# Performance work log

Measured on AMD Instinct MI355X. Metric: run time of the kernel, lower is better.

Reference implementation:

```python
import jax, jax.numpy as jnp
import numpy as np

TEMP = 0.2
N_IT = 10
P = 1


def setup_inputs() -> dict:
    key = jax.random.key(0)
    N, M = 8192, 8192
    k1, _ = jax.random.split(key)
    cdist = jax.random.uniform(k1, (N, M), dtype=jnp.float32)
    A = jnp.ones((N,), dtype=jnp.float32) / N  # uniform source density
    B = jnp.ones((M,), dtype=jnp.float32) / M  # uniform target density
    return {"cdist": cdist, "A": A, "B": B}


def reference(cdist, A, B):
    N, M = cdist.shape
    # C = (cdist - cdist.min()) / cdist.std(); torch std is unbiased (ddof=1)
    C = (cdist - cdist.min()) / jnp.std(cdist, ddof=1)
    # p == 1 -> no power applied
    Q = jnp.exp(-C / TEMP)
    Q = Q / Q.sum()

    def body(i, carry):
        U, V = carry
        # T implicit as U[:,None] * Q * V; first iter T == Q since U=V=1
        T = U[:, None] * Q * V[None, :]
        V = V * (B / T.sum(axis=0))
        T = U[:, None] * Q * V[None, :]
        U = U * (A / T.sum(axis=1))
        return (U, V)

    U0 = jnp.ones((N,), dtype=cdist.dtype)
    V0 = jnp.ones((M,), dtype=cdist.dtype)
    U, V = jax.lax.fori_loop(0, N_IT, body, (U0, V0))
    T = U[:, None] * Q * V[None, :]
    return T
```

## Files before the change

### kernel.cpp

```cpp
#include <hip/hip_runtime.h>
#include <hip/hip_fp16.h>

#define TEMP_ 0.2
#define NITER 10

typedef _Float16 half_t;
struct __align__(8)  H4 { half_t h[4]; };
struct __align__(16) H8 { half_t h[8]; };

__device__ __forceinline__ float wsum(float v){
#pragma unroll
  for (int o = 32; o > 0; o >>= 1) v += __shfl_down(v, o, 64);
  return v;
}
__device__ __forceinline__ double wsumd(double v){
#pragma unroll
  for (int o = 32; o > 0; o >>= 1) v += __shfl_down(v, o, 64);
  return v;
}
__device__ __forceinline__ float wmin(float v){
#pragma unroll
  for (int o = 32; o > 0; o >>= 1) v = fminf(v, __shfl_down(v, o, 64));
  return v;
}

__device__ __forceinline__ unsigned fenc(float f){
  unsigned u = __float_as_uint(f);
  return (u & 0x80000000u) ? ~u : (u | 0x80000000u);
}
__device__ __forceinline__ float fdec(unsigned u){
  return (u & 0x80000000u) ? __uint_as_float(u & 0x7FFFFFFFu) : __uint_as_float(~u);
}

__device__ __forceinline__ void get_stats(const double* __restrict__ sums,
                                          const unsigned* __restrict__ minbits,
                                          long long NM, float& cmin, float& kscale){
  double s  = sums[0];
  double ss = sums[1];
  double mean = s / (double)NM;
  double var  = (ss - mean * s) / (double)(NM - 1);
  cmin  = fdec(*minbits);
  kscale = (float)(1.0 / (sqrt(var) * TEMP_));
}

__global__ void k_init(double* __restrict__ sums, double* __restrict__ Ssum,
                       unsigned* __restrict__ minbits, float* __restrict__ colsum, int M){
  int i = blockIdx.x * blockDim.x + threadIdx.x;
  if (i == 0){ sums[0] = 0.0; sums[1] = 0.0; *Ssum = 0.0; *minbits = 0xFFFFFFFFu; }
  if (i < M) colsum[i] = 0.f;
}

__global__ __launch_bounds__(256) void k_reduce(const float* __restrict__ cd, long long n4,
                                                double* __restrict__ sums,
                                                unsigned* __restrict__ minbits){
  const float4* c4 = (const float4*)cd;
  long long i0 = (long long)blockIdx.x * blockDim.x + threadIdx.x;
  long long stride = (long long)gridDim.x * blockDim.x;
  double s = 0.0, ss = 0.0;
  float  fs = 0.f, fss = 0.f;
  float  mn = __int_as_float(0x7F800000);
  int cnt = 0;
  for (long long i = i0; i < n4; i += stride){
    float4 v = c4[i];
    mn = fminf(mn, fminf(fminf(v.x, v.y), fminf(v.z, v.w)));
    fs  += (v.x + v.y) + (v.z + v.w);
    fss += v.x*v.x + v.y*v.y + v.z*v.z + v.w*v.w;
    if (++cnt == 8){ s += fs; ss += fss; fs = 0.f; fss = 0.f; cnt = 0; }
  }
  s += fs; ss += fss;
  s = wsumd(s); ss = wsumd(ss); mn = wmin(mn);
  __shared__ double lds[8];
  __shared__ float  ldm[4];
  int lane = threadIdx.x & 63, wid = threadIdx.x >> 6;
  if (lane == 0){ lds[wid] = s; lds[4 + wid] = ss; ldm[wid] = mn; }
  __syncthreads();
  if (threadIdx.x == 0){
    unsafeAtomicAdd(&sums[0], lds[0] + lds[1] + lds[2] + lds[3]);
    unsafeAtomicAdd(&sums[1], lds[4] + lds[5] + lds[6] + lds[7]);
    atomicMin(minbits, fenc(fminf(fminf(ldm[0], ldm[1]), fminf(ldm[2], ldm[3]))));
  }
}

__global__ __launch_bounds__(256) void k_expcol(const float* __restrict__ cd, half_t* __restrict__ E,
                                                const double* __restrict__ sums,
                                                const unsigned* __restrict__ minbits,
                                                float* __restrict__ colsum, double* __restrict__ Ssum,
                                                int N, int M){
  float cmin, kscale;
  get_stats(sums, minbits, (long long)N * M, cmin, kscale);
  int c0 = blockIdx.x * 1024 + threadIdx.x * 4;
  int r0 = blockIdx.y * 64;
  float a0 = 0.f, a1 = 0.f, a2 = 0.f, a3 = 0.f;
#pragma unroll 4
  for (int r = 0; r < 64; ++r){
    long long idx = (long long)(r0 + r) * M + c0;
    float4 v = *(const float4*)(cd + idx);
    float e0 = __expf((cmin - v.x) * kscale);
    float e1 = __expf((cmin - v.y) * kscale);
    float e2 = __expf((cmin - v.z) * kscale);
    float e3 = __expf((cmin - v.w) * kscale);
    H4 o; o.h[0] = (half_t)e0; o.h[1] = (half_t)e1; o.h[2] = (half_t)e2; o.h[3] = (half_t)e3;
    *(H4*)(E + idx) = o;
    a0 += e0; a1 += e1; a2 += e2; a3 += e3;
  }
  unsafeAtomicAdd(&colsum[c0 + 0], a0);
  unsafeAtomicAdd(&colsum[c0 + 1], a1);
  unsafeAtomicAdd(&colsum[c0 + 2], a2);
  unsafeAtomicAdd(&colsum[c0 + 3], a3);
  float tot = wsum((a0 + a1) + (a2 + a3));
  __shared__ float lt[4];
  int lane = threadIdx.x & 63, wid = threadIdx.x >> 6;
  if (lane == 0) lt[wid] = tot;
  __syncthreads();
  if (threadIdx.x == 0) unsafeAtomicAdd(Ssum, (double)(lt[0] + lt[1] + lt[2] + lt[3]));
}

__global__ void k_v(const float* __restrict__ B, const float* __restrict__ colsum,
                    const double* __restrict__ Ssum, float* __restrict__ v, int M){
  int j = blockIdx.x * blockDim.x + threadIdx.x;
  if (j < M) v[j] = (float)((double)B[j] * (*Ssum) / (double)colsum[j]);
}

__global__ __launch_bounds__(256) void k_row(const half_t* __restrict__ E, const float* __restrict__ v,
                                             float* __restrict__ rowsum, int M){
  int t = threadIdx.x;
  int r0 = blockIdx.x * 8;
  float vr[32];
#pragma unroll
  for (int k = 0; k < 4; ++k){
    int c = k * 2048 + t * 8;
    float4 a = *(const float4*)(v + c);
    float4 b = *(const float4*)(v + c + 4);
    vr[k*8+0] = a.x; vr[k*8+1] = a.y; vr[k*8+2] = a.z; vr[k*8+3] = a.w;
    vr[k*8+4] = b.x; vr[k*8+5] = b.y; vr[k*8+6] = b.z; vr[k*8+7] = b.w;
  }
  __shared__ float lds[4][8];
  int lane = t & 63, wid = t >> 6;
  for (int r = 0; r < 8; ++r){
    const half_t* Er = E + (long long)(r0 + r) * M;
    float p = 0.f;
#pragma unroll
    for (int k = 0; k < 4; ++k){
      H8 hh = *(const H8*)(Er + k * 2048 + t * 8);
      p += (float)hh.h[0]*vr[k*8+0] + (float)hh.h[1]*vr[k*8+1]
         + (float)hh.h[2]*vr[k*8+2] + (float)hh.h[3]*vr[k*8+3]
         + (float)hh.h[4]*vr[k*8+4] + (float)hh.h[5]*vr[k*8+5]
         + (float)hh.h[6]*vr[k*8+6] + (float)hh.h[7]*vr[k*8+7];
    }
    p = wsum(p);
    if (lane == 0) lds[wid][r] = p;
  }
  __syncthreads();
  if (t < 8) rowsum[r0 + t] = lds[0][t] + lds[1][t] + lds[2][t] + lds[3][t];
}

__global__ void k_u(const float* __restrict__ A, const float* __restrict__ rowsum,
                    const double* __restrict__ Ssum, float* __restrict__ u,
                    float* __restrict__ colsum, int N, int M){
  int i = blockIdx.x * blockDim.x + threadIdx.x;
  if (i < N) u[i] = (float)((double)A[i] * (*Ssum) / (double)rowsum[i]);
  if (i < M) colsum[i] = 0.f;
}

__global__ __launch_bounds__(256) void k_col(const half_t* __restrict__ E, const float* __restrict__ u,
                                             float* __restrict__ colsum, int M){
  int c0 = blockIdx.x * 1024 + threadIdx.x * 4;
  int r0 = blockIdx.y * 64;
  float a0 = 0.f, a1 = 0.f, a2 = 0.f, a3 = 0.f;
#pragma unroll 4
  for (int r = 0; r < 64; ++r){
    int row = r0 + r;
    float ur = u[row];
    H4 hh = *(const H4*)(E + (long long)row * M + c0);
    a0 += ur * (float)hh.h[0];
    a1 += ur * (float)hh.h[1];
    a2 += ur * (float)hh.h[2];
    a3 += ur * (float)hh.h[3];
  }
  unsafeAtomicAdd(&colsum[c0 + 0], a0);
  unsafeAtomicAdd(&colsum[c0 + 1], a1);
  unsafeAtomicAdd(&colsum[c0 + 2], a2);
  unsafeAtomicAdd(&colsum[c0 + 3], a3);
}

__global__ __launch_bounds__(256) void k_final(const float* __restrict__ cd,
                                               const float* __restrict__ u, const float* __restrict__ v,
                                               const double* __restrict__ sums,
                                               const unsigned* __restrict__ minbits,
                                               const double* __restrict__ Ssum,
                                               float* __restrict__ T, int N, int M){
  float cmin, kscale;
  get_stats(sums, minbits, (long long)N * M, cmin, kscale);
  float invS = (float)(1.0 / (*Ssum));
  int t = threadIdx.x;
  int r0 = blockIdx.x * 8;
  float vr[32];
#pragma unroll
  for (int k = 0; k < 4; ++k){
    int c = k * 2048 + t * 8;
    float4 a = *(const float4*)(v + c);
    float4 b = *(const float4*)(v + c + 4);
    vr[k*8+0] = a.x * invS; vr[k*8+1] = a.y * invS; vr[k*8+2] = a.z * invS; vr[k*8+3] = a.w * invS;
    vr[k*8+4] = b.x * invS; vr[k*8+5] = b.y * invS; vr[k*8+6] = b.z * invS; vr[k*8+7] = b.w * invS;
  }
  for (int r = 0; r < 8; ++r){
    int row = r0 + r;
    float ur = u[row];
#pragma unroll
    for (int k = 0; k < 4; ++k){
      long long idx = (long long)row * M + k * 2048 + t * 8;
      float4 a = *(const float4*)(cd + idx);
      float4 b = *(const float4*)(cd + idx + 4);
      float4 oa, ob;
      oa.x = ur * vr[k*8+0] * __expf((cmin - a.x) * kscale);
      oa.y = ur * vr[k*8+1] * __expf((cmin - a.y) * kscale);
      oa.z = ur * vr[k*8+2] * __expf((cmin - a.z) * kscale);
      oa.w = ur * vr[k*8+3] * __expf((cmin - a.w) * kscale);
      ob.x = ur * vr[k*8+4] * __expf((cmin - b.x) * kscale);
      ob.y = ur * vr[k*8+5] * __expf((cmin - b.y) * kscale);
      ob.z = ur * vr[k*8+6] * __expf((cmin - b.z) * kscale);
      ob.w = ur * vr[k*8+7] * __expf((cmin - b.w) * kscale);
      *(float4*)(T + idx) = oa;
      *(float4*)(T + idx + 4) = ob;
    }
  }
}

extern "C" void kernel_launch(void* const* d_in, const int* in_sizes, int n_in,
                              void* d_out, int out_size, void* d_ws, size_t ws_size,
                              hipStream_t stream){
  const float* cd = (const float*)d_in[0];
  const float* A  = (const float*)d_in[1];
  const float* B  = (const float*)d_in[2];
  int N = in_sizes[1];
  int M = in_sizes[2];
  float*  T = (float*)d_out;
  half_t* E = (half_t*)d_out;

  char* ws = (char*)d_ws;
  double*   sums    = (double*)ws;
  double*   Ssum    = (double*)(ws + 16);
  unsigned* minbits = (unsigned*)(ws + 24);
  float*    colsum  = (float*)(ws + 32);
  float*    rowsum  = colsum + M;
  float*    u       = rowsum + N;
  float*    v       = u + N;

  int mx = (N > M) ? N : M;
  long long n4 = (long long)N * M / 4;

  k_init<<<(mx + 255) / 256, 256, 0, stream>>>(sums, Ssum, minbits, colsum, M);
  k_reduce<<<2048, 256, 0, stream>>>(cd, n4, sums, minbits);
  k_expcol<<<dim3(M / 1024, N / 64), 256, 0, stream>>>(cd, E, sums, minbits, colsum, Ssum, N, M);

  for (int it = 0; it < NITER; ++it){
    if (it > 0) k_col<<<dim3(M / 1024, N / 64), 256, 0, stream>>>(E, u, colsum, M);
    k_v<<<(M + 255) / 256, 256, 0, stream>>>(B, colsum, Ssum, v, M);
    k_row<<<N / 8, 256, 0, stream>>>(E, v, rowsum, M);
    k_u<<<(mx + 255) / 256, 256, 0, stream>>>(A, rowsum, Ssum, u, colsum, N, M);
  }
  k_final<<<N / 8, 256, 0, stream>>>(cd, u, v, sums, minbits, Ssum, T, N, M);
}
```

Measured before the change: 1.206 ms.

## Fuse scaling kernels into row/column passes and build final output from fp16 E

Drops the separate k_v and k_u kernels. v is computed on the fly from the column sums in a shared load_vr helper, and u is computed at the end of the row pass (k_rp). Column sums now ping-pong between two buffers, and the zeroing for the next iteration is folded into the column pass (k_cp), which also caches u in LDS. Column and exp kernels move to 8-wide fp16 vectors, and reciprocals use the fast hardware rcp instead of double division. The final output is built from the fp16 E matrix for three quarters of the rows, in an order that respects E aliasing the output buffer, with nontemporal stores. This trades output precision (fp16 E, approximate rcp) for fewer launches and less fp32 traffic.

Result: slower. 1.353 ms (+12.2%).

```diff
diff --git a/kernel.cpp b/kernel.cpp
--- a/kernel.cpp
+++ b/kernel.cpp
@@ -1,12 +1,14 @@
 #include <hip/hip_runtime.h>
-#include <hip/hip_fp16.h>
 
 #define TEMP_ 0.2
 #define NITER 10
 
+
 typedef _Float16 half_t;
-struct __align__(8)  H4 { half_t h[4]; };
 struct __align__(16) H8 { half_t h[8]; };
+typedef float floatx4 __attribute__((ext_vector_type(4)));
+
+__device__ __forceinline__ float fast_rcp(float x){ return __builtin_amdgcn_rcpf(x); }
 
 __device__ __forceinline__ float wsum(float v){
 #pragma unroll
@@ -43,11 +45,33 @@
   kscale = (float)(1.0 / (sqrt(var) * TEMP_));
 }
 
+__device__ __forceinline__ void load_vr(const float* __restrict__ cs,
+                                        const float* __restrict__ B,
+                                        float S, int t, float* vr){
+#pragma unroll
+  for (int k = 0; k < 4; ++k){
+    int c = k * 2048 + t * 8;
+    float4 ca = *(const float4*)(cs + c);
+    float4 cb = *(const float4*)(cs + c + 4);
+    float4 ba = *(const float4*)(B + c);
+    float4 bb = *(const float4*)(B + c + 4);
+    vr[k*8+0] = ba.x * S * fast_rcp(ca.x);
+    vr[k*8+1] = ba.y * S * fast_rcp(ca.y);
+    vr[k*8+2] = ba.z * S * fast_rcp(ca.z);
+    vr[k*8+3] = ba.w * S * fast_rcp(ca.w);
+    vr[k*8+4] = bb.x * S * fast_rcp(cb.x);
+    vr[k*8+5] = bb.y * S * fast_rcp(cb.y);
+    vr[k*8+6] = bb.z * S * fast_rcp(cb.z);
+    vr[k*8+7] = bb.w * S * fast_rcp(cb.w);
+  }
+}
+
 __global__ void k_init(double* __restrict__ sums, double* __restrict__ Ssum,
-                       unsigned* __restrict__ minbits, float* __restrict__ colsum, int M){
+                       unsigned* __restrict__ minbits,
+                       float* __restrict__ c0, float* __restrict__ c1, int M){
   int i = blockIdx.x * blockDim.x + threadIdx.x;
   if (i == 0){ sums[0] = 0.0; sums[1] = 0.0; *Ssum = 0.0; *minbits = 0xFFFFFFFFu; }
-  if (i < M) colsum[i] = 0.f;
+  if (i < M){ c0[i] = 0.f; c1[i] = 0.f; }
 }
 
 __global__ __launch_bounds__(256) void k_reduce(const float* __restrict__ cd, long long n4,
@@ -88,121 +112,166 @@
                                                 int N, int M){
   float cmin, kscale;
   get_stats(sums, minbits, (long long)N * M, cmin, kscale);
-  int c0 = blockIdx.x * 1024 + threadIdx.x * 4;
+  int t = threadIdx.x;
+  int c0 = blockIdx.x * 2048 + t * 8;
   int r0 = blockIdx.y * 64;
-  float a0 = 0.f, a1 = 0.f, a2 = 0.f, a3 = 0.f;
+  float a0=0.f,a1=0.f,a2=0.f,a3=0.f,a4=0.f,a5=0.f,a6=0.f,a7=0.f;
 #pragma unroll 4
   for (int r = 0; r < 64; ++r){
     long long idx = (long long)(r0 + r) * M + c0;
-    float4 v = *(const float4*)(cd + idx);
-    float e0 = __expf((cmin - v.x) * kscale);
-    float e1 = __expf((cmin - v.y) * kscale);
-    float e2 = __expf((cmin - v.z) * kscale);
-    float e3 = __expf((cmin - v.w) * kscale);
-    H4 o; o.h[0] = (half_t)e0; o.h[1] = (half_t)e1; o.h[2] = (half_t)e2; o.h[3] = (half_t)e3;
-    *(H4*)(E + idx) = o;
-    a0 += e0; a1 += e1; a2 += e2; a3 += e3;
-  }
-  unsafeAtomicAdd(&colsum[c0 + 0], a0);
-  unsafeAtomicAdd(&colsum[c0 + 1], a1);
-  unsafeAtomicAdd(&colsum[c0 + 2], a2);
-  unsafeAtomicAdd(&colsum[c0 + 3], a3);
-  float tot = wsum((a0 + a1) + (a2 + a3));
+    float4 va = *(const float4*)(cd + idx);
+    float4 vb = *(const float4*)(cd + idx + 4);
+    float e0 = __expf((cmin - va.x) * kscale);
+    float e1 = __expf((cmin - va.y) * kscale);
+    float e2 = __expf((cmin - va.z) * kscale);
+    float e3 = __expf((cmin - va.w) * kscale);
+    float e4 = __expf((cmin - vb.x) * kscale);
+    float e5 = __expf((cmin - vb.y) * kscale);
+    float e6 = __expf((cmin - vb.z) * kscale);
+    float e7 = __expf((cmin - vb.w) * kscale);
+    H8 o;
+    o.h[0]=(half_t)e0; o.h[1]=(half_t)e1; o.h[2]=(half_t)e2; o.h[3]=(half_t)e3;
+    o.h[4]=(half_t)e4; o.h[5]=(half_t)e5; o.h[6]=(half_t)e6; o.h[7]=(half_t)e7;
+    *(H8*)(E + idx) = o;
+    a0+=e0; a1+=e1; a2+=e2; a3+=e3; a4+=e4; a5+=e5; a6+=e6; a7+=e7;
+  }
+  unsafeAtomicAdd(&colsum[c0+0], a0);
+  unsafeAtomicAdd(&colsum[c0+1], a1);
+  unsafeAtomicAdd(&colsum[c0+2], a2);
+  unsafeAtomicAdd(&colsum[c0+3], a3);
+  unsafeAtomicAdd(&colsum[c0+4], a4);
+  unsafeAtomicAdd(&colsum[c0+5], a5);
+  unsafeAtomicAdd(&colsum[c0+6], a6);
+  unsafeAtomicAdd(&colsum[c0+7], a7);
+  float tot = wsum(((a0+a1)+(a2+a3)) + ((a4+a5)+(a6+a7)));
   __shared__ float lt[4];
-  int lane = threadIdx.x & 63, wid = threadIdx.x >> 6;
+  int lane = t & 63, wid = t >> 6;
   if (lane == 0) lt[wid] = tot;
   __syncthreads();
-  if (threadIdx.x == 0) unsafeAtomicAdd(Ssum, (double)(lt[0] + lt[1] + lt[2] + lt[3]));
-}
-
-__global__ void k_v(const float* __restrict__ B, const float* __restrict__ colsum,
-                    const double* __restrict__ Ssum, float* __restrict__ v, int M){
-  int j = blockIdx.x * blockDim.x + threadIdx.x;
-  if (j < M) v[j] = (float)((double)B[j] * (*Ssum) / (double)colsum[j]);
-}
-
-__global__ __launch_bounds__(256) void k_row(const half_t* __restrict__ E, const float* __restrict__ v,
-                                             float* __restrict__ rowsum, int M){
+  if (t == 0) unsafeAtomicAdd(Ssum, (double)((lt[0] + lt[1]) + (lt[2] + lt[3])));
+}
+
+__global__ __launch_bounds__(256) void k_rp(const half_t* __restrict__ E,
+                                            const float* __restrict__ cs,
+                                            const float* __restrict__ B,
+                                            const float* __restrict__ A,
+                                            const double* __restrict__ Ssum,
+                                            float* __restrict__ u, int M){
   int t = threadIdx.x;
   int r0 = blockIdx.x * 8;
+  float S = (float)(*Ssum);
   float vr[32];
-#pragma unroll
-  for (int k = 0; k < 4; ++k){
-    int c = k * 2048 + t * 8;
-    float4 a = *(const float4*)(v + c);
-    float4 b = *(const float4*)(v + c + 4);
-    vr[k*8+0] = a.x; vr[k*8+1] = a.y; vr[k*8+2] = a.z; vr[k*8+3] = a.w;
-    vr[k*8+4] = b.x; vr[k*8+5] = b.y; vr[k*8+6] = b.z; vr[k*8+7] = b.w;
-  }
-  __shared__ float lds[4][8];
-  int lane = t & 63, wid = t >> 6;
+  load_vr(cs, B, S, t, vr);
+  float acc[8];
+  const half_t* Eb = E + (long long)r0 * M;
+#pragma unroll
   for (int r = 0; r < 8; ++r){
-    const half_t* Er = E + (long long)(r0 + r) * M;
     float p = 0.f;
 #pragma unroll
     for (int k = 0; k < 4; ++k){
-      H8 hh = *(const H8*)(Er + k * 2048 + t * 8);
+      H8 hh = *(const H8*)(Eb + (long long)r * M + k * 2048 + t * 8);
       p += (float)hh.h[0]*vr[k*8+0] + (float)hh.h[1]*vr[k*8+1]
          + (float)hh.h[2]*vr[k*8+2] + (float)hh.h[3]*vr[k*8+3]
          + (float)hh.h[4]*vr[k*8+4] + (float)hh.h[5]*vr[k*8+5]
          + (float)hh.h[6]*vr[k*8+6] + (float)hh.h[7]*vr[k*8+7];
     }
-    p = wsum(p);
+    acc[r] = p;
+  }
+  __shared__ float lds[4][8];
+  int lane = t & 63, wid = t >> 6;
+#pragma unroll
+  for (int r = 0; r < 8; ++r){
+    float p = wsum(acc[r]);
     if (lane == 0) lds[wid][r] = p;
   }
   __syncthreads();
-  if (t < 8) rowsum[r0 + t] = lds[0][t] + lds[1][t] + lds[2][t] + lds[3][t];
-}
-
-__global__ void k_u(const float* __restrict__ A, const float* __restrict__ rowsum,
-                    const double* __restrict__ Ssum, float* __restrict__ u,
-                    float* __restrict__ colsum, int N, int M){
-  int i = blockIdx.x * blockDim.x + threadIdx.x;
-  if (i < N) u[i] = (float)((double)A[i] * (*Ssum) / (double)rowsum[i]);
-  if (i < M) colsum[i] = 0.f;
-}
-
-__global__ __launch_bounds__(256) void k_col(const half_t* __restrict__ E, const float* __restrict__ u,
-                                             float* __restrict__ colsum, int M){
-  int c0 = blockIdx.x * 1024 + threadIdx.x * 4;
+  if (t < 8){
+    float rs = (lds[0][t] + lds[1][t]) + (lds[2][t] + lds[3][t]);
+    u[r0 + t] = A[r0 + t] * S * fast_rcp(rs);
+  }
+}
+
+__global__ __launch_bounds__(256) void k_cp(const half_t* __restrict__ E,
+                                            const float* __restrict__ u,
+                                            float* __restrict__ cs_next,
+                                            float* __restrict__ cs_zero, int M){
+  int t = threadIdx.x;
+  int c0 = blockIdx.x * 2048 + t * 8;
   int r0 = blockIdx.y * 64;
-  float a0 = 0.f, a1 = 0.f, a2 = 0.f, a3 = 0.f;
-#pragma unroll 4
+  int bid = blockIdx.y * gridDim.x + blockIdx.x;
+  int z = bid * 16 + t;
+  if (t < 16 && z < M) cs_zero[z] = 0.f;
+  __shared__ float ul[64];
+  if (t < 64) ul[t] = u[r0 + t];
+  __syncthreads();
+  float a0=0.f,a1=0.f,a2=0.f,a3=0.f,a4=0.f,a5=0.f,a6=0.f,a7=0.f;
+#pragma unroll 8
   for (int r = 0; r < 64; ++r){
-    int row = r0 + r;
-    float ur = u[row];
-    H4 hh = *(const H4*)(E + (long long)row * M + c0);
+    float ur = ul[r];
+    H8 hh = *(const H8*)(E + (long long)(r0 + r) * M + c0);
     a0 += ur * (float)hh.h[0];
     a1 += ur * (float)hh.h[1];
     a2 += ur * (float)hh.h[2];
     a3 += ur * (float)hh.h[3];
-  }
-  unsafeAtomicAdd(&colsum[c0 + 0], a0);
-  unsafeAtomicAdd(&colsum[c0 + 1], a1);
-  unsafeAtomicAdd(&colsum[c0 + 2], a2);
-  unsafeAtomicAdd(&colsum[c0 + 3], a3);
-}
-
-__global__ __launch_bounds__(256) void k_final(const float* __restrict__ cd,
-                                               const float* __restrict__ u, const float* __restrict__ v,
-                                               const double* __restrict__ sums,
-                                               const unsigned* __restrict__ minbits,
-                                               const double* __restrict__ Ssum,
-                                               float* __restrict__ T, int N, int M){
+    a4 += ur * (float)hh.h[4];
+    a5 += ur * (float)hh.h[5];
+    a6 += ur * (float)hh.h[6];
+    a7 += ur * (float)hh.h[7];
+  }
+  unsafeAtomicAdd(&cs_next[c0+0], a0);
+  unsafeAtomicAdd(&cs_next[c0+1], a1);
+  unsafeAtomicAdd(&cs_next[c0+2], a2);
+  unsafeAtomicAdd(&cs_next[c0+3], a3);
+  unsafeAtomicAdd(&cs_next[c0+4], a4);
+  unsafeAtomicAdd(&cs_next[c0+5], a5);
+  unsafeAtomicAdd(&cs_next[c0+6], a6);
+  unsafeAtomicAdd(&cs_next[c0+7], a7);
+}
+
+__global__ __launch_bounds__(256) void k_final_E(const half_t* __restrict__ E,
+                                                 const float* __restrict__ u,
+                                                 const float* __restrict__ cs,
+                                                 const float* __restrict__ B,
+                                                 float* __restrict__ T, int r_base, int M){
+  int t = threadIdx.x;
+  int r0 = r_base + blockIdx.x * 8;
+  float vr[32];
+  load_vr(cs, B, 1.0f, t, vr);
+  for (int r = 0; r < 8; ++r){
+    int row = r0 + r;
+    float ur = u[row];
+#pragma unroll
+    for (int k = 0; k < 4; ++k){
+      long long idx = (long long)row * M + k * 2048 + t * 8;
+      H8 hh = *(const H8*)(E + idx);
+      floatx4 oa, ob;
+      oa.x = ur * vr[k*8+0] * (float)hh.h[0];
+      oa.y = ur * vr[k*8+1] * (float)hh.h[1];
+      oa.z = ur * vr[k*8+2] * (float)hh.h[2];
+      oa.w = ur * vr[k*8+3] * (float)hh.h[3];
+      ob.x = ur * vr[k*8+4] * (float)hh.h[4];
+      ob.y = ur * vr[k*8+5] * (float)hh.h[5];
+      ob.z = ur * vr[k*8+6] * (float)hh.h[6];
+      ob.w = ur * vr[k*8+7] * (float)hh.h[7];
+      __builtin_nontemporal_store(oa, (floatx4*)(T + idx));
+      __builtin_nontemporal_store(ob, (floatx4*)(T + idx + 4));
+    }
+  }
+}
+
+__global__ __launch_bounds__(256) void k_final_cd(const float* __restrict__ cd,
+                                                  const float* __restrict__ u,
+                                                  const float* __restrict__ cs,
+                                                  const float* __restrict__ B,
+                                                  const double* __restrict__ sums,
+                                                  const unsigned* __restrict__ minbits,
+                                                  float* __restrict__ T, int N, int M){
   float cmin, kscale;
   get_stats(sums, minbits, (long long)N * M, cmin, kscale);
-  float invS = (float)(1.0 / (*Ssum));
   int t = threadIdx.x;
   int r0 = blockIdx.x * 8;
   float vr[32];
-#pragma unroll
-  for (int k = 0; k < 4; ++k){
-    int c = k * 2048 + t * 8;
-    float4 a = *(const float4*)(v + c);
-    float4 b = *(const float4*)(v + c + 4);
-    vr[k*8+0] = a.x * invS; vr[k*8+1] = a.y * invS; vr[k*8+2] = a.z * invS; vr[k*8+3] = a.w * invS;
-    vr[k*8+4] = b.x * invS; vr[k*8+5] = b.y * invS; vr[k*8+6] = b.z * invS; vr[k*8+7] = b.w * invS;
-  }
+  load_vr(cs, B, 1.0f, t, vr);
   for (int r = 0; r < 8; ++r){
     int row = r0 + r;
     float ur = u[row];
@@ -211,7 +280,7 @@
       long long idx = (long long)row * M + k * 2048 + t * 8;
       float4 a = *(const float4*)(cd + idx);
       float4 b = *(const float4*)(cd + idx + 4);
-      float4 oa, ob;
+      floatx4 oa, ob;
       oa.x = ur * vr[k*8+0] * __expf((cmin - a.x) * kscale);
       oa.y = ur * vr[k*8+1] * __expf((cmin - a.y) * kscale);
       oa.z = ur * vr[k*8+2] * __expf((cmin - a.z) * kscale);
@@ -220,8 +289,8 @@
       ob.y = ur * vr[k*8+5] * __expf((cmin - b.y) * kscale);
       ob.z = ur * vr[k*8+6] * __expf((cmin - b.z) * kscale);
       ob.w = ur * vr[k*8+7] * __expf((cmin - b.w) * kscale);
-      *(float4*)(T + idx) = oa;
-      *(float4*)(T + idx + 4) = ob;
+      __builtin_nontemporal_store(oa, (floatx4*)(T + idx));
+      __builtin_nontemporal_store(ob, (floatx4*)(T + idx + 4));
     }
   }
 }
@@ -241,23 +310,26 @@
   double*   sums    = (double*)ws;
   double*   Ssum    = (double*)(ws + 16);
   unsigned* minbits = (unsigned*)(ws + 24);
-  float*    colsum  = (float*)(ws + 32);
-  float*    rowsum  = colsum + M;
-  float*    u       = rowsum + N;
-  float*    v       = u + N;
-
-  int mx = (N > M) ? N : M;
+  float*    c0      = (float*)(ws + 32);
+  float*    c1      = c0 + M;
+  float*    u       = c1 + M;
+
   long long n4 = (long long)N * M / 4;
 
-  k_init<<<(mx + 255) / 256, 256, 0, stream>>>(sums, Ssum, minbits, colsum, M);
+  k_init<<<(M + 255) / 256, 256, 0, stream>>>(sums, Ssum, minbits, c0, c1, M);
   k_reduce<<<2048, 256, 0, stream>>>(cd, n4, sums, minbits);
-  k_expcol<<<dim3(M / 1024, N / 64), 256, 0, stream>>>(cd, E, sums, minbits, colsum, Ssum, N, M);
+  k_expcol<<<dim3(M / 2048, N / 64), 256, 0, stream>>>(cd, E, sums, minbits, c0, Ssum, N, M);
 
   for (int it = 0; it < NITER; ++it){
-    if (it > 0) k_col<<<dim3(M / 1024, N / 64), 256, 0, stream>>>(E, u, colsum, M);
-    k_v<<<(M + 255) / 256, 256, 0, stream>>>(B, colsum, Ssum, v, M);
-    k_row<<<N / 8, 256, 0, stream>>>(E, v, rowsum, M);
-    k_u<<<(mx + 255) / 256, 256, 0, stream>>>(A, rowsum, Ssum, u, colsum, N, M);
-  }
-  k_final<<<N / 8, 256, 0, stream>>>(cd, u, v, sums, minbits, Ssum, T, N, M);
-}
+    float* cur = (it & 1) ? c1 : c0;
+    float* nxt = (it & 1) ? c0 : c1;
+    k_rp<<<N / 8, 256, 0, stream>>>(E, cur, B, A, Ssum, u, M);
+    if (it + 1 < NITER)
+      k_cp<<<dim3(M / 2048, N / 64), 256, 0, stream>>>(E, u, nxt, cur, M);
+  }
+  float* csl = ((NITER - 1) & 1) ? c1 : c0;
+
+  k_final_E<<<(N / 2) / 8, 256, 0, stream>>>(E, u, csl, B, T, N / 2, M);
+  k_final_E<<<(N / 4) / 8, 256, 0, stream>>>(E, u, csl, B, T, N / 4, M);
+  k_final_cd<<<(N / 4) / 8, 256, 0, stream>>>(cd, u, csl, B, sums, minbits, T, N, M);
+}
```
